# Kernel tuning notes

Measured on AMD Instinct MI355X. Metric: run time of the kernel, lower is better.

## Reference

```python
import jax, jax.numpy as jnp
import numpy as np

B, N, NPOINT, NSAMPLE = 16, 4096, 1024, 32
IN_CH = 3
MLP = [64, 64, 128]
EPS = 1e-5


def setup_inputs() -> dict:
    key = jax.random.key(0)
    ks = jax.random.split(key, 16)
    inp = {
        "xyz": jax.random.normal(ks[0], (B, N, 3), jnp.float32),
        "points": jax.random.normal(ks[1], (B, N, IN_CH), jnp.float32),
        "fps_idx": jax.random.randint(ks[2], (B, NPOINT), 0, N, jnp.int64),
    }
    last = IN_CH + 3
    for li, out_ch in enumerate(MLP):
        kw, kb, kg, kt = jax.random.split(jax.random.fold_in(key, 100 + li), 4)
        inp[f"w{li}"] = jax.random.normal(kw, (out_ch, last), jnp.float32) * (1.0 / np.sqrt(last))
        inp[f"b{li}"] = jax.random.normal(kb, (out_ch,), jnp.float32) * 0.01
        inp[f"g{li}"] = 1.0 + 0.1 * jax.random.normal(kg, (out_ch,), jnp.float32)
        inp[f"t{li}"] = 0.1 * jax.random.normal(kt, (out_ch,), jnp.float32)
        last = out_ch
    return inp


def _gather(x, idx):
    # x: [B, N, C], idx: [B, ...] -> [B, ..., C]
    return jax.vmap(lambda xb, ib: xb[ib])(x, idx)


def _conv_bn_relu(x, w, b, g, t):
    # x: [B, S, K, Cin]; 1x1 conv == channel matmul; BN in training mode (batch stats)
    y = jnp.einsum('bskc,oc->bsko', x, w) + b
    mean = y.mean(axis=(0, 1, 2))
    var = y.var(axis=(0, 1, 2))  # biased, as torch BN uses for normalization
    y = (y - mean) * jax.lax.rsqrt(var + EPS) * g + t
    return jax.nn.relu(y)


def reference(xyz, points, fps_idx, w0, b0, g0, t0, w1, b1, g1, t1, w2, b2, g2, t2):
    # sample query points
    new_xyz = jnp.take_along_axis(xyz, fps_idx[..., None], axis=1)  # [B, S, 3]
    # kNN ball query: squared distances [B, S, N]
    d = (jnp.sum(new_xyz**2, -1)[:, :, None]
         + jnp.sum(xyz**2, -1)[:, None, :]
         - 2.0 * jnp.einsum('bsd,bnd->bsn', new_xyz, xyz))
    _, idx = jax.lax.top_k(-d, NSAMPLE)  # [B, S, K]
    grouped_xyz = _gather(xyz, idx)                      # [B, S, K, 3]
    normed = grouped_xyz - new_xyz[:, :, None, :]
    grouped_pts = _gather(points, idx)                   # [B, S, K, Cin]
    x = jnp.concatenate([normed, grouped_pts], axis=-1)  # [B, S, K, 3+Cin]
    x = _conv_bn_relu(x, w0, b0, g0, t0)
    x = _conv_bn_relu(x, w1, b1, g1, t1)
    x = _conv_bn_relu(x, w2, b2, g2, t2)
    feat = jnp.max(x, axis=2)  # max over nsample -> [B, S, Cout]
    return (new_xyz, feat)
```

## Files before the change

### kernel.cpp

```cpp
#include <hip/hip_runtime.h>

#define BB 16
#define NN 4096
#define SS 1024
#define KK 32
#define MPTS (BB*SS*KK)
#define EPSF 1e-5f
#define CANDCAP 512
#define WNARROW 16

#define OFF_QP    0
#define OFF_P4    (OFF_QP + BB*SS*4)
#define OFF_ST    (OFF_P4 + BB*NN*4)
#define OFF_MOM   (OFF_ST)
#define OFF_S1SUM (OFF_ST+32)
#define OFF_S1SQ  (OFF_ST+96)
#define OFF_S2SUM (OFF_ST+160)
#define OFF_S2SQ  (OFF_ST+288)
#define OFF_XG    (OFF_ST+1280)
#define OFF_MAXB  (OFF_XG + 6*MPTS)
#define OFF_MINB  (OFF_MAXB + BB*SS*128)
#define OFF_Y1U   (OFF_MINB + BB*SS*128)

typedef __bf16 bf16x8 __attribute__((ext_vector_type(8)));
typedef float f32x4 __attribute__((ext_vector_type(4)));
typedef unsigned int uintx4 __attribute__((ext_vector_type(4)));

__device__ __forceinline__ unsigned rne_bf16(float f){
  unsigned u = __float_as_uint(f);
  return (u + 0x7FFFu + ((u>>16)&1u)) >> 16;
}

__global__ __launch_bounds__(256) void prep_kernel(
    const float* __restrict__ xyz, const int* __restrict__ fps,
    float* __restrict__ out, float* __restrict__ ws)
{
  const int g = blockIdx.x*256 + threadIdx.x;
  if (g < BB*NN){
    const float* p = xyz + (size_t)g*3;
    float x=p[0], y=p[1], z=p[2];
    float x2 = __fadd_rn(__fadd_rn(__fmul_rn(x,x),__fmul_rn(y,y)),__fmul_rn(z,z));
    *reinterpret_cast<float4*>(ws + OFF_P4 + (size_t)g*4) = make_float4(x,y,z,x2);
  } else {
    int j = g - BB*NN;
    if (j < BB*SS){
      int b = j >> 10;
      int idx = fps[j];
      const float* p = xyz + ((size_t)b*NN + idx)*3;
      float x=p[0], y=p[1], z=p[2];
      out[(size_t)j*3+0]=x; out[(size_t)j*3+1]=y; out[(size_t)j*3+2]=z;
      float q2 = __fadd_rn(__fadd_rn(__fmul_rn(x,x),__fmul_rn(y,y)),__fmul_rn(z,z));
      *reinterpret_cast<float4*>(ws + OFF_QP + (size_t)j*4) = make_float4(x,y,z,q2);
    }
  }
}

__global__ __launch_bounds__(256) void knn_group_kernel(
    const float* __restrict__ pts, float* __restrict__ ws)
{
  __shared__ unsigned long long cand[CANDCAP];
  __shared__ int sel[KK];
  __shared__ unsigned sh_mcnt;

  const int bid = blockIdx.x;
  const int b = bid >> 10;
  const int tid = threadIdx.x;

  const float4 q = *reinterpret_cast<const float4*>(ws + OFF_QP + (size_t)bid*4);
  const float qx=q.x, qy=q.y, qz=q.z, q2=q.w;
  const float4* pb = reinterpret_cast<const float4*>(ws + OFF_P4) + (size_t)b*NN;

  float d[16];
  #pragma unroll
  for (int j=0;j<16;j++){
    int n = tid + j*256;
    float4 P = pb[n];
    float dot = __fadd_rn(__fadd_rn(__fmul_rn(qx,P.x),__fmul_rn(qy,P.y)),__fmul_rn(qz,P.z));
    d[j] = __fsub_rn(__fadd_rn(q2, P.w), __fmul_rn(2.0f,dot));
  }

  if (tid==0) sh_mcnt = 0;

  float mn = d[0], mx = d[0];
  #pragma unroll
  for (int j=1;j<16;j++){ mn = fminf(mn,d[j]); mx = fmaxf(mx,d[j]); }
  #pragma unroll
  for (int off=32; off>=1; off>>=1){
    mn = fminf(mn, __shfl_xor(mn, off, 64));
    mx = fmaxf(mx, __shfl_xor(mx, off, 64));
  }

  float lo = mn, hi = __int_as_float(0x7F800000);
  unsigned clo = 0, chi = 1024;
  int rounds = 0;
  while (chi - clo > WNARROW && rounds < 24){
    float mid;
    if (rounds == 0){
      mid = mx;
    } else if (rounds < 8){
      float frac = (float)(KK - (int)clo) / (float)(chi - clo);
      mid = lo + (hi - lo) * exp2f(0.6666667f * log2f(frac));
    } else {
      mid = 0.5f*lo + 0.5f*hi;
    }
    if (!(mid > lo && mid < hi)) mid = 0.5f*lo + 0.5f*hi;
    if (!(mid > lo && mid < hi)) break;
    unsigned cnt = 0;
    #pragma unroll
    for (int j=0;j<16;j++)
      cnt += (unsigned)__popcll(__ballot((int)(d[j] < mid)));
    if (cnt >= (unsigned)KK){ hi = mid; chi = cnt; } else { lo = mid; clo = cnt; }
    ++rounds;
  }
  __syncthreads();

  #pragma unroll
  for (int j=0;j<16;j++){
    if (d[j] < hi){
      unsigned u = __float_as_uint(d[j]);
      unsigned key = u ^ (unsigned)(((int)u>>31) | (int)0x80000000);
      unsigned p = atomicAdd(&sh_mcnt,1u);
      if (p < CANDCAP) cand[p] = ((unsigned long long)key<<32) | (unsigned)(tid + j*256);
    }
  }
  __syncthreads();
  const unsigned m = (sh_mcnt < CANDCAP) ? sh_mcnt : CANDCAP;
  for (unsigned i=tid; i<m; i+=256){
    const unsigned long long ci = cand[i];
    unsigned r = 0;
    #pragma unroll 4
    for (unsigned jj=0; jj<m; ++jj) r += (cand[jj] < ci) ? 1u : 0u;
    if (r < (unsigned)KK) sel[(int)r] = (int)(ci & 0xFFFFFFFFu);
  }
  __syncthreads();

  if (tid < KK){
    int n = sel[tid];
    float4 P = pb[n];
    float v6[6];
    v6[0] = P.x-qx; v6[1] = P.y-qy; v6[2] = P.z-qz;
    const float* pt = pts + ((size_t)b*NN + n)*3;
    v6[3] = pt[0]; v6[4] = pt[1]; v6[5] = pt[2];
    size_t pidx = (size_t)bid*KK + tid;
    float* xg = ws + OFF_XG;
    #pragma unroll
    for (int c=0;c<6;c++) xg[(size_t)c*MPTS + pidx] = v6[c];
  }
}

__global__ __launch_bounds__(256) void mom2_kernel(float* __restrict__ ws)
{
  static const signed char C1[27]={0,1,2,3,4,5, 0,0,0,0,0,0, 1,1,1,1,1, 2,2,2,2, 3,3,3, 4,4, 5};
  static const signed char C2[27]={-1,-1,-1,-1,-1,-1, 0,1,2,3,4,5, 1,2,3,4,5, 2,3,4,5, 3,4,5, 4,5, 5};
  const int mq = blockIdx.x >> 3;
  const int sl = blockIdx.x & 7;
  const float4* xa = reinterpret_cast<const float4*>(ws + OFF_XG + (size_t)C1[mq]*MPTS) + (size_t)sl*(MPTS/32);
  const int c2 = C2[mq];
  float s = 0.f;
  if (c2 < 0){
    for (int i=threadIdx.x; i<MPTS/32; i+=256){
      float4 a = xa[i];
      s += (a.x+a.y)+(a.z+a.w);
    }
  } else {
    const float4* xb = reinterpret_cast<const float4*>(ws + OFF_XG + (size_t)c2*MPTS) + (size_t)sl*(MPTS/32);
    for (int i=threadIdx.x; i<MPTS/32; i+=256){
      float4 a = xa[i]; float4 bq = xb[i];
      s = fmaf(a.x,bq.x,s); s = fmaf(a.y,bq.y,s);
      s = fmaf(a.z,bq.z,s); s = fmaf(a.w,bq.w,s);
    }
  }
  #pragma unroll
  for (int off=32; off>=1; off>>=1) s += __shfl_xor(s,off,64);
  __shared__ float r[4];
  const int lane = threadIdx.x & 63, wv = threadIdx.x >> 6;
  if (lane==0) r[wv]=s;
  __syncthreads();
  if (threadIdx.x==0) atomicAdd(&ws[OFF_MOM+mq], r[0]+r[1]+r[2]+r[3]);
}

__global__ __launch_bounds__(256) void l1_mfma_kernel(
    const float* __restrict__ w0g, const float* __restrict__ b0g,
    const float* __restrict__ g0, const float* __restrict__ t0,
    const float* __restrict__ w1g, const float* __restrict__ b1g,
    float* __restrict__ ws)
{
  __shared__ __align__(16) unsigned short sA1[4096];
  __shared__ float swf[64*8];
  __shared__ float red[128];
  const int tid = threadIdx.x;
  const int lane = tid & 63;
  const int wv = tid >> 6;
  const int col = lane & 15;
  const int kg = lane >> 4;

  for (int idx=tid; idx<4096; idx+=256){
    int frag = idx>>9, l = (idx>>3)&63, j = idx&7;
    int mt = frag>>1, kt = frag&1;
    int o = mt*16 + (l&15);
    int c = kt*32 + ((l>>4)<<3) + j;
    sA1[idx] = (unsigned short)rne_bf16(w1g[o*64+c]);
  }
  if (tid<64){
    const float* mom = ws + OFF_MOM;
    float w[6];
    #pragma unroll
    for (int c=0;c<6;c++) w[c] = w0g[tid*6+c];
    float bo = b0g[tid];
    float wS = 0.f;
    #pragma unroll
    for (int c=0;c<6;c++) wS += w[c]*mom[c];
    const float Mf = (float)MPTS;
    float mean = (wS + Mf*bo) / Mf;
    float qsum = 0.f;
    int mi = 6;
    #pragma unroll
    for (int c=0;c<6;c++){
      #pragma unroll
      for (int c2=c;c2<6;c2++){
        float f = (c==c2)?1.f:2.f;
        qsum += f * w[c]*w[c2]*mom[mi];
        mi++;
      }
    }
    float E2  = (qsum + 2.f*bo*wS + Mf*bo*bo) / Mf;
    float var = E2 - mean*mean;
    float sc  = g0[tid] / sqrtf(var + EPSF);
    float sh  = t0[tid] - mean*sc;
    #pragma unroll
    for (int c=0;c<6;c++) swf[tid*8+c] = sc*w[c];
    swf[tid*8+6] = sc*bo + sh;
    swf[tid*8+7] = 0.f;
  }
  if (tid<128) red[tid]=0.f;
  __syncthreads();

  float cw0[2][8], cw1[2][8], cw2[2][8], cw3[2][8], cw4[2][8], cw5[2][8], cb[2][8];
  #pragma unroll
  for (int kt=0; kt<2; ++kt){
    #pragma unroll
    for (int j=0;j<8;j++){
      int c = kt*32 + kg*8 + j;
      float4 a4 = *reinterpret_cast<const float4*>(&swf[c*8]);
      float4 b4 = *reinterpret_cast<const float4*>(&swf[c*8 + 4]);
      cw0[kt][j]=a4.x; cw1[kt][j]=a4.y; cw2[kt][j]=a4.z; cw3[kt][j]=a4.w;
      cw4[kt][j]=b4.x; cw5[kt][j]=b4.y; cb[kt][j]=b4.z;
    }
  }
  float b1v[4][4];
  #pragma unroll
  for (int mt=0;mt<4;mt++)
    #pragma unroll
    for (int r=0;r<4;r++) b1v[mt][r] = b1g[mt*16 + kg*4 + r];

  float s1s[4][4], s1q[4][4];
  #pragma unroll
  for (int mt=0;mt<4;mt++)
    #pragma unroll
    for (int r=0;r<4;r++){ s1s[mt][r]=0.f; s1q[mt][r]=0.f; }

  const float* xg = ws + OFF_XG;
  unsigned short* y1 = (unsigned short*)(ws + OFF_Y1U);
  const int pbase = (blockIdx.x*4 + wv)*256;

  for (int it=0; it<16; ++it){
    const size_t p = (size_t)pbase + it*16 + col;
    const float x0 = xg[p];
    const float x1 = xg[MPTS+p];
    const float x2 = xg[2ul*MPTS+p];
    const float x3 = xg[3ul*MPTS+p];
    const float x4 = xg[4ul*MPTS+p];
    const float x5 = xg[5ul*MPTS+p];

    f32x4 acc0 = {0,0,0,0}, acc1 = {0,0,0,0}, acc2 = {0,0,0,0}, acc3 = {0,0,0,0};

    #pragma unroll
    for (int kt=0; kt<2; ++kt){
      float h[8];
      #pragma unroll
      for (int j=0;j<8;j++){
        float y = cb[kt][j];
        y = fmaf(cw0[kt][j],x0,y); y = fmaf(cw1[kt][j],x1,y);
        y = fmaf(cw2[kt][j],x2,y); y = fmaf(cw3[kt][j],x3,y);
        y = fmaf(cw4[kt][j],x4,y); y = fmaf(cw5[kt][j],x5,y);
        h[j] = fmaxf(y, 0.f);
      }
      uintx4 pk;
      pk[0] = rne_bf16(h[0]) | (rne_bf16(h[1])<<16);
      pk[1] = rne_bf16(h[2]) | (rne_bf16(h[3])<<16);
      pk[2] = rne_bf16(h[4]) | (rne_bf16(h[5])<<16);
      pk[3] = rne_bf16(h[6]) | (rne_bf16(h[7])<<16);
      bf16x8 bfrag = __builtin_bit_cast(bf16x8, pk);
      {
        uintx4 au = *reinterpret_cast<const uintx4*>(&sA1[((0*2+kt)*64+lane)*8]);
        acc0 = __builtin_amdgcn_mfma_f32_16x16x32_bf16(__builtin_bit_cast(bf16x8,au), bfrag, acc0, 0,0,0);
      }
      {
        uintx4 au = *reinterpret_cast<const uintx4*>(&sA1[((1*2+kt)*64+lane)*8]);
        acc1 = __builtin_amdgcn_mfma_f32_16x16x32_bf16(__builtin_bit_cast(bf16x8,au), bfrag, acc1, 0,0,0);
      }
      {
        uintx4 au = *reinterpret_cast<const uintx4*>(&sA1[((2*2+kt)*64+lane)*8]);
        acc2 = __builtin_amdgcn_mfma_f32_16x16x32_bf16(__builtin_bit_cast(bf16x8,au), bfrag, acc2, 0,0,0);
      }
      {
        uintx4 au = *reinterpret_cast<const uintx4*>(&sA1[((3*2+kt)*64+lane)*8]);
        acc3 = __builtin_amdgcn_mfma_f32_16x16x32_bf16(__builtin_bit_cast(bf16x8,au), bfrag, acc3, 0,0,0);
      }
    }
    #pragma unroll
    for (int mt=0;mt<4;mt++){
      f32x4 a = (mt==0)?acc0:(mt==1)?acc1:(mt==2)?acc2:acc3;
      float v0 = a[0] + b1v[mt][0];
      float v1 = a[1] + b1v[mt][1];
      float v2 = a[2] + b1v[mt][2];
      float v3 = a[3] + b1v[mt][3];
      s1s[mt][0]+=v0; s1q[mt][0]=fmaf(v0,v0,s1q[mt][0]);
      s1s[mt][1]+=v1; s1q[mt][1]=fmaf(v1,v1,s1q[mt][1]);
      s1s[mt][2]+=v2; s1q[mt][2]=fmaf(v2,v2,s1q[mt][2]);
      s1s[mt][3]+=v3; s1q[mt][3]=fmaf(v3,v3,s1q[mt][3]);
      uint2 st;
      st.x = rne_bf16(v0) | (rne_bf16(v1)<<16);
      st.y = rne_bf16(v2) | (rne_bf16(v3)<<16);
      *reinterpret_cast<uint2*>(y1 + p*64 + mt*16 + kg*4) = st;
    }
  }

  #pragma unroll
  for (int mt=0;mt<4;mt++){
    #pragma unroll
    for (int r=0;r<4;r++){
      float s = s1s[mt][r], qv = s1q[mt][r];
      s += __shfl_xor(s,1,64); s += __shfl_xor(s,2,64);
      s += __shfl_xor(s,4,64); s += __shfl_xor(s,8,64);
      qv += __shfl_xor(qv,1,64); qv += __shfl_xor(qv,2,64);
      qv += __shfl_xor(qv,4,64); qv += __shfl_xor(qv,8,64);
      if (col==0){
        atomicAdd(&red[mt*16 + kg*4 + r], s);
        atomicAdd(&red[64 + mt*16 + kg*4 + r], qv);
      }
    }
  }
  __syncthreads();
  if (tid < 64){
    atomicAdd(&ws[OFF_S1SUM+tid], red[tid]);
    atomicAdd(&ws[OFF_S1SQ+tid],  red[64+tid]);
  }
}

__global__ __launch_bounds__(256) void l2_mfma_kernel(
    const float* __restrict__ w2g, const float* __restrict__ b2g,
    const float* __restrict__ g1, const float* __restrict__ t1,
    float* __restrict__ ws)
{
  __shared__ __align__(16) unsigned short sB[8192];
  __shared__ float s1c[64], s1h[64];
  __shared__ float red[256];
  const int tid = threadIdx.x;
  for (int idx=tid; idx<8192; idx+=256){
    int nt = idx>>10, kt = (idx>>9)&1, l = (idx>>3)&63, j = idx&7;
    int kch = kt*32 + ((l>>4)<<3) + j;
    int o   = (nt<<4) + (l&15);
    sB[idx] = (unsigned short)rne_bf16(w2g[o*64+kch]);
  }
  if (tid<64){
    const float Mf = (float)MPTS;
    float mean = ws[OFF_S1SUM+tid]/Mf;
    float var  = ws[OFF_S1SQ+tid]/Mf - mean*mean;
    float sc = g1[tid]/sqrtf(var+EPSF);
    s1c[tid]=sc; s1h[tid]=t1[tid]-mean*sc;
  }
  red[tid]=0.f;
  __syncthreads();

  const int lane = tid & 63;
  const int w    = tid >> 6;
  const int col  = lane & 15;
  const int kg   = lane >> 4;

  float scv[2][8], shv[2][8];
  #pragma unroll
  for (int kt=0;kt<2;kt++)
    #pragma unroll
    for (int j=0;j<8;j++){
      scv[kt][j] = s1c[kt*32 + kg*8 + j];
      shv[kt][j] = s1h[kt*32 + kg*8 + j];
    }
  float b2v[8];
  #pragma unroll
  for (int nt=0;nt<8;nt++) b2v[nt] = b2g[nt*16 + col];

  const unsigned short* y1 = (const unsigned short*)(ws + OFF_Y1U);
  float* maxb = ws + OFF_MAXB;
  float* minb = ws + OFF_MINB;

  float sumacc[8], sqacc[8];
  #pragma unroll
  for (int nt=0;nt<8;nt++){ sumacc[nt]=0.f; sqacc[nt]=0.f; }

  const int gbase = (blockIdx.x*4 + w)*4;
  for (int it=0; it<4; ++it){
    const int g = gbase + it;
    const size_t p0 = (size_t)g*32;
    bf16x8 aA[2][2];
    #pragma unroll
    for (int mh=0; mh<2; ++mh){
      const unsigned short* arow = y1 + (p0 + mh*16 + col)*64 + kg*8;
      #pragma unroll
      for (int kt=0; kt<2; ++kt){
        uintx4 ua = *reinterpret_cast<const uintx4*>(arow + kt*32);
        float h0 = fmaxf(fmaf(scv[kt][0], __uint_as_float(ua[0]<<16),          shv[kt][0]), 0.f);
        float h1 = fmaxf(fmaf(scv[kt][1], __uint_as_float(ua[0]&0xFFFF0000u), shv[kt][1]), 0.f);
        float h2 = fmaxf(fmaf(scv[kt][2], __uint_as_float(ua[1]<<16),          shv[kt][2]), 0.f);
        float h3 = fmaxf(fmaf(scv[kt][3], __uint_as_float(ua[1]&0xFFFF0000u), shv[kt][3]), 0.f);
        float h4 = fmaxf(fmaf(scv[kt][4], __uint_as_float(ua[2]<<16),          shv[kt][4]), 0.f);
        float h5 = fmaxf(fmaf(scv[kt][5], __uint_as_float(ua[2]&0xFFFF0000u), shv[kt][5]), 0.f);
        float h6 = fmaxf(fmaf(scv[kt][6], __uint_as_float(ua[3]<<16),          shv[kt][6]), 0.f);
        float h7 = fmaxf(fmaf(scv[kt][7], __uint_as_float(ua[3]&0xFFFF0000u), shv[kt][7]), 0.f);
        uintx4 pk;
        pk[0] = rne_bf16(h0) | (rne_bf16(h1)<<16);
        pk[1] = rne_bf16(h2) | (rne_bf16(h3)<<16);
        pk[2] = rne_bf16(h4) | (rne_bf16(h5)<<16);
        pk[3] = rne_bf16(h6) | (rne_bf16(h7)<<16);
        aA[mh][kt] = __builtin_bit_cast(bf16x8, pk);
      }
    }
    f32x4 acc[2][8];
    #pragma unroll
    for (int mh=0;mh<2;mh++)
      #pragma unroll
      for (int nt=0;nt<8;nt++){
        f32x4 z = {b2v[nt], b2v[nt], b2v[nt], b2v[nt]};
        acc[mh][nt] = z;
      }
    #pragma unroll
    for (int nt=0;nt<8;nt++){
      #pragma unroll
      for (int kt=0;kt<2;kt++){
        uintx4 bu = *reinterpret_cast<const uintx4*>(&sB[((nt*2+kt)*64 + lane)*8]);
        bf16x8 bv = __builtin_bit_cast(bf16x8, bu);
        acc[0][nt] = __builtin_amdgcn_mfma_f32_16x16x32_bf16(aA[0][kt], bv, acc[0][nt], 0,0,0);
        acc[1][nt] = __builtin_amdgcn_mfma_f32_16x16x32_bf16(aA[1][kt], bv, acc[1][nt], 0,0,0);
      }
    }
    #pragma unroll
    for (int nt=0;nt<8;nt++){
      f32x4 a0 = acc[0][nt], a1 = acc[1][nt];
      float mx = fmaxf(fmaxf(fmaxf(a0[0],a0[1]),fmaxf(a0[2],a0[3])),
                       fmaxf(fmaxf(a1[0],a1[1]),fmaxf(a1[2],a1[3])));
      float mn = fminf(fminf(fminf(a0[0],a0[1]),fminf(a0[2],a0[3])),
                       fminf(fminf(a1[0],a1[1]),fminf(a1[2],a1[3])));
      mx = fmaxf(mx, __shfl_xor(mx,16,64)); mx = fmaxf(mx, __shfl_xor(mx,32,64));
      mn = fminf(mn, __shfl_xor(mn,16,64)); mn = fminf(mn, __shfl_xor(mn,32,64));
      float s = ((a0[0]+a0[1])+(a0[2]+a0[3])) + ((a1[0]+a1[1])+(a1[2]+a1[3]));
      sumacc[nt] += s;
      float qv = 0.f;
      qv = fmaf(a0[0],a0[0],qv); qv = fmaf(a0[1],a0[1],qv);
      qv = fmaf(a0[2],a0[2],qv); qv = fmaf(a0[3],a0[3],qv);
      qv = fmaf(a1[0],a1[0],qv); qv = fmaf(a1[1],a1[1],qv);
      qv = fmaf(a1[2],a1[2],qv); qv = fmaf(a1[3],a1[3],qv);
      sqacc[nt] += qv;
      if (lane < 16){
        maxb[(size_t)g*128 + nt*16 + lane] = mx;
        minb[(size_t)g*128 + nt*16 + lane] = mn;
      }
    }
  }
  #pragma unroll
  for (int nt=0;nt<8;nt++){
    float s = sumacc[nt]; s += __shfl_xor(s,16,64); s += __shfl_xor(s,32,64);
    float qv = sqacc[nt]; qv += __shfl_xor(qv,16,64); qv += __shfl_xor(qv,32,64);
    if (lane < 16){
      atomicAdd(&red[nt*16+lane], s);
      atomicAdd(&red[128+nt*16+lane], qv);
    }
  }
  __syncthreads();
  atomicAdd(&ws[OFF_S2SUM + tid], red[tid]);
}

__global__ __launch_bounds__(256) void final_out_kernel(
    const float* __restrict__ g2, const float* __restrict__ t2,
    const float* __restrict__ ws, float* __restrict__ out)
{
  const int g = blockIdx.x*256 + threadIdx.x;
  const int o = g & 127;
  const float Mf = (float)MPTS;
  float mean = ws[OFF_S2SUM+o] / Mf;
  float var  = ws[OFF_S2SQ+o] / Mf - mean*mean;
  float sc = g2[o] / sqrtf(var + EPSF);
  float sh = t2[o] - mean*sc;
  float v = (sc > 0.f) ? ws[OFF_MAXB+g] : ws[OFF_MINB+g];
  out[BB*SS*3 + g] = fmaxf(fmaf(sc, v, sh), 0.f);
}

extern "C" void kernel_launch(void* const* d_in, const int* in_sizes, int n_in,
                              void* d_out, int out_size, void* d_ws, size_t ws_size,
                              hipStream_t stream)
{
  const float* xyz = (const float*)d_in[0];
  const float* pts = (const float*)d_in[1];
  const int*   fps = (const int*)d_in[2];
  const float* w0  = (const float*)d_in[3];
  const float* b0  = (const float*)d_in[4];
  const float* g0  = (const float*)d_in[5];
  const float* t0  = (const float*)d_in[6];
  const float* w1  = (const float*)d_in[7];
  const float* b1  = (const float*)d_in[8];
  const float* g1  = (const float*)d_in[9];
  const float* t1  = (const float*)d_in[10];
  const float* w2  = (const float*)d_in[11];
  const float* b2  = (const float*)d_in[12];
  const float* g2  = (const float*)d_in[13];
  const float* t2  = (const float*)d_in[14];
  float* out = (float*)d_out;
  float* ws  = (float*)d_ws;

  hipMemsetAsync((void*)(ws + OFF_ST), 0, 512*sizeof(float), stream);
  prep_kernel<<<320,256,0,stream>>>(xyz, fps, out, ws);
  knn_group_kernel<<<BB*SS,256,0,stream>>>(pts, ws);
  mom2_kernel<<<27*8,256,0,stream>>>(ws);
  l1_mfma_kernel<<<512,256,0,stream>>>(w0,b0,g0,t0,w1,b1,ws);
  l2_mfma_kernel<<<1024,256,0,stream>>>(w2,b2,g1,t1,ws);
  final_out_kernel<<<(BB*SS*128)/256,256,0,stream>>>(g2,t2,ws,out);
}
```

Before: 261.9 us.

## Use block-wide kNN threshold search with cubic-volume interpolation

The kNN radius search now reduces min/max and per-round ballot counts across all four waves through shared memory, so one threshold is found for the whole block instead of one per wave. The interpolation step guesses the next threshold by interpolating counts in d^1.5 space, which models uniform point density in 3D. A looser stop width is allowed. The aim is fewer candidates in the following rank-sort stage and fewer search rounds. The cost is a __syncthreads and shared-memory reduction in every search round.

```diff
diff --git a/kernel.cpp b/kernel.cpp
--- a/kernel.cpp
+++ b/kernel.cpp
@@ -7,7 +7,7 @@
 #define MPTS (BB*SS*KK)
 #define EPSF 1e-5f
 #define CANDCAP 512
-#define WNARROW 16
+#define NARROW 48
 
 #define OFF_QP    0
 #define OFF_P4    (OFF_QP + BB*SS*4)
@@ -29,6 +29,10 @@
 __device__ __forceinline__ unsigned rne_bf16(float f){
   unsigned u = __float_as_uint(f);
   return (u + 0x7FFFu + ((u>>16)&1u)) >> 16;
+}
+
+__device__ __forceinline__ float pow15(float v){
+  return exp2f(1.5f * log2f(fmaxf(v, 1e-30f)));
 }
 
 __global__ __launch_bounds__(256) void prep_kernel(
@@ -58,6 +62,8 @@
 __global__ __launch_bounds__(256) void knn_group_kernel(
     const float* __restrict__ pts, float* __restrict__ ws)
 {
+  __shared__ unsigned wcnt[2][4];
+  __shared__ float wmm[4][2];
   __shared__ unsigned long long cand[CANDCAP];
   __shared__ int sel[KK];
   __shared__ unsigned sh_mcnt;
@@ -65,6 +71,8 @@
   const int bid = blockIdx.x;
   const int b = bid >> 10;
   const int tid = threadIdx.x;
+  const int lane = tid & 63;
+  const int wv = tid >> 6;
 
   const float4 q = *reinterpret_cast<const float4*>(ws + OFF_QP + (size_t)bid*4);
   const float qx=q.x, qy=q.y, qz=q.z, q2=q.w;
@@ -89,27 +97,35 @@
     mn = fminf(mn, __shfl_xor(mn, off, 64));
     mx = fmaxf(mx, __shfl_xor(mx, off, 64));
   }
-
-  float lo = mn, hi = __int_as_float(0x7F800000);
-  unsigned clo = 0, chi = 1024;
+  if (lane==0){ wmm[wv][0]=mn; wmm[wv][1]=mx; }
+  __syncthreads();
+  mn = fminf(fminf(wmm[0][0],wmm[1][0]),fminf(wmm[2][0],wmm[3][0]));
+  mx = fmaxf(fmaxf(wmm[0][1],wmm[1][1]),fmaxf(wmm[2][1],wmm[3][1]));
+
+  float lo = mn, hi = mx*1.0001f + 1e-6f;
+  unsigned clo = 0, chi = NN;
   int rounds = 0;
-  while (chi - clo > WNARROW && rounds < 24){
+  while (chi - clo > NARROW && rounds < 20){
     float mid;
-    if (rounds == 0){
-      mid = mx;
-    } else if (rounds < 8){
-      float frac = (float)(KK - (int)clo) / (float)(chi - clo);
-      mid = lo + (hi - lo) * exp2f(0.6666667f * log2f(frac));
+    if (rounds < 10){
+      float pl = pow15(lo), ph = pow15(hi);
+      float t = (float)(KK - (int)clo) / (float)(chi - clo);
+      float target = fmaf(t, ph - pl, pl);
+      mid = exp2f(0.6666667f * log2f(fmaxf(target, 1e-30f)));
     } else {
-      mid = 0.5f*lo + 0.5f*hi;
-    }
-    if (!(mid > lo && mid < hi)) mid = 0.5f*lo + 0.5f*hi;
+      mid = 0.5f*(lo + hi);
+    }
+    if (!(mid > lo && mid < hi)) mid = 0.5f*(lo + hi);
     if (!(mid > lo && mid < hi)) break;
     unsigned cnt = 0;
     #pragma unroll
     for (int j=0;j<16;j++)
       cnt += (unsigned)__popcll(__ballot((int)(d[j] < mid)));
-    if (cnt >= (unsigned)KK){ hi = mid; chi = cnt; } else { lo = mid; clo = cnt; }
+    if (lane==0) wcnt[rounds&1][wv] = cnt;
+    __syncthreads();
+    const unsigned c = wcnt[rounds&1][0]+wcnt[rounds&1][1]
+                     + wcnt[rounds&1][2]+wcnt[rounds&1][3];
+    if (c >= (unsigned)KK){ hi = mid; chi = c; } else { lo = mid; clo = c; }
     ++rounds;
   }
   __syncthreads();
```

Result: faster. 218.9 us (-16.4%).
